# Performance work log

Measured on AMD Instinct MI355X. Metric: run time of the kernel, lower is better.

The kernel has to match this reference:

```python
import jax, jax.numpy as jnp
import numpy as np

EMBED_DIM = 768
Q_DIM = 64
V_DIM = 64
WINDOW_SIZE = 3


def setup_inputs() -> dict:
    key = jax.random.key(0)
    ks = jax.random.split(key, 7)
    B, N = 4, 4096
    s = 1.0 / np.sqrt(EMBED_DIM)
    x = jax.random.normal(ks[0], (B, N, EMBED_DIM), dtype=jnp.float32)
    Wq = jax.random.normal(ks[1], (EMBED_DIM, Q_DIM), dtype=jnp.float32) * s
    bq = jax.random.normal(ks[2], (Q_DIM,), dtype=jnp.float32) * 0.01
    Wk = jax.random.normal(ks[3], (EMBED_DIM, Q_DIM), dtype=jnp.float32) * s
    bk = jax.random.normal(ks[4], (Q_DIM,), dtype=jnp.float32) * 0.01
    Wv = jax.random.normal(ks[5], (EMBED_DIM, V_DIM), dtype=jnp.float32) * s
    bv = jax.random.normal(ks[6], (V_DIM,), dtype=jnp.float32) * 0.01
    return {"x": x, "Wq": Wq, "bq": bq, "Wk": Wk, "bk": bk, "Wv": Wv, "bv": bv}


def reference(x, Wq, bq, Wk, bk, Wv, bv):
    # Faithful translation of SliddingWindowAttention.forward, including the
    # original's quirk: diagonal scores are written into columns 0..window_size-1
    # of a full (B, N, N) zero matrix, softmax is taken over ALL N columns
    # (zeros included), and the result is matmul'd with V.
    B, N, _ = x.shape
    Q = x @ Wq + bq  # (B, N, Q_DIM)
    K = x @ Wk + bk  # (B, N, Q_DIM)
    V = x @ Wv + bv  # (B, N, V_DIM)

    half = WINDOW_SIZE // 2
    columns = jnp.zeros((B, N, N), dtype=x.dtype)
    for idx, di in enumerate(range(-half, half + 1)):
        # diagonal offset di: pair row i with column j = i + di (valid rows only)
        rows = np.arange(max(0, -di), N - max(0, di))
        cols_j = rows + di
        c = jnp.einsum('bid,bid->bi', Q[:, rows, :], K[:, cols_j, :])
        columns = columns.at[:, rows, idx].set(c)

    attn = jax.nn.softmax(columns, axis=2)  # (B, N, N)
    return attn @ V  # (B, N, V_DIM)
```

## Files before the change

### kernel.cpp

```cpp
#include <hip/hip_runtime.h>
#include <hip/hip_bf16.h>
#include <math.h>

#define EMBED 768
#define NTOK  4096
#define NB    4
#define ROWS  16384
#define CN    192

typedef __attribute__((ext_vector_type(8))) short bf16x8;
typedef __attribute__((ext_vector_type(8))) unsigned short u16x8;
typedef __attribute__((ext_vector_type(4))) float f32x4;

__device__ inline void split2(float f, short& h, short& l) {
  union { float f; unsigned u; } a; a.f = f;
  unsigned r = (a.u + 0x7FFFu + ((a.u >> 16) & 1u)) & 0xFFFF0000u;
  h = (short)(r >> 16);
  union { unsigned u; float f; } hf; hf.u = r;
  union { float f; unsigned u; } b; b.f = f - hf.f;
  l = (short)((b.u + 0x7FFFu + ((b.u >> 16) & 1u)) >> 16);
}

__global__ __launch_bounds__(256) void wprep(const float* __restrict__ Wq,
                                             const float* __restrict__ Wk,
                                             const float* __restrict__ Wv,
                                             unsigned short* __restrict__ Wt,
                                             float* __restrict__ Vsum) {
  __shared__ float tile[32 * 64];
  const int b   = blockIdx.x;
  const int mat = b / 24;
  const int ks  = b - mat * 24;
  const float* W = (mat == 0) ? Wq : (mat == 1) ? Wk : Wv;
  const int t = threadIdx.x;

  const float4* src = (const float4*)(W + ks * 2048);
  ((float4*)tile)[t]       = src[t];
  ((float4*)tile)[t + 256] = src[t + 256];
  __syncthreads();

  const int q    = t >> 6;
  const int nloc = t & 63;
  u16x8 hv, lv;
#pragma unroll
  for (int j = 0; j < 8; ++j) {
    short h, l;
    split2(tile[(q * 8 + j) * 64 + nloc], h, l);
    hv[j] = (unsigned short)h;
    lv[j] = (unsigned short)l;
  }
  const size_t base = (size_t)ks * 12288 + (size_t)q * 1536 + (size_t)(mat * 64 + nloc) * 8;
  *(u16x8*)(Wt + base)        = hv;
  *(u16x8*)(Wt + base + 6144) = lv;

  if (b == 0 && t < NB * 64) Vsum[t] = 0.f;
}


__device__ inline void splitHW(float f, short& h, short& l) {
  __hip_bfloat16 hb = __float2bfloat16(f);
  float hf = __bfloat162float(hb);
  __hip_bfloat16 lb = __float2bfloat16(f - hf);
  h = __builtin_bit_cast(short, hb);
  l = __builtin_bit_cast(short, lb);
}

__device__ inline void cvt8hw(const float4 f0, const float4 f1, bf16x8& h, bf16x8& l) {
  short hh, ll;
  splitHW(f0.x, hh, ll); h[0] = hh; l[0] = ll;
  splitHW(f0.y, hh, ll); h[1] = hh; l[1] = ll;
  splitHW(f0.z, hh, ll); h[2] = hh; l[2] = ll;
  splitHW(f0.w, hh, ll); h[3] = hh; l[3] = ll;
  splitHW(f1.x, hh, ll); h[4] = hh; l[4] = ll;
  splitHW(f1.y, hh, ll); h[5] = hh; l[5] = ll;
  splitHW(f1.z, hh, ll); h[6] = hh; l[6] = ll;
  splitHW(f1.w, hh, ll); h[7] = hh; l[7] = ll;
}

__global__ __launch_bounds__(512, 6) void qkv_mfma(const float* __restrict__ x,
                                                   const unsigned short* __restrict__ Wtu,
                                                   const float* __restrict__ bq,
                                                   const float* __restrict__ bk,
                                                   const float* __restrict__ bv,
                                                   float* __restrict__ C,
                                                   float* __restrict__ Vsum) {
  __shared__ float ms[4][16][48];

  const int tid  = threadIdx.x;
  const int lane = tid & 63;
  const int wv   = tid >> 6;
  const int wn   = wv >> 1;
  const int kh   = wv & 1;
  const int ml   = lane & 15;
  const int q    = lane >> 4;
  const int r0   = blockIdx.x * 16;

  f32x4 acc0 = {0.f,0.f,0.f,0.f}, acc1 = {0.f,0.f,0.f,0.f}, acc2 = {0.f,0.f,0.f,0.f};

  const float*          xa = x   + (size_t)(r0 + ml) * EMBED + kh * 384 + q * 8;
  const unsigned short* Bb = Wtu + (size_t)(kh * 12) * 12288 + q * 1536 + (wn * 48 + ml) * 8;

  for (int ks = 0; ks < 12; ++ks) {
    const bf16x8* bp = (const bf16x8*)Bb;
    bf16x8 bh0 = bp[0],  bl0 = bp[768];
    bf16x8 bh1 = bp[16], bl1 = bp[784];
    bf16x8 bh2 = bp[32], bl2 = bp[800];
    float4 a0 = *(const float4*)xa;
    float4 a1 = *(const float4*)(xa + 4);
    bf16x8 ah, al;
    cvt8hw(a0, a1, ah, al);
    acc0 = __builtin_amdgcn_mfma_f32_16x16x32_bf16(ah, bh0, acc0, 0, 0, 0);
    acc1 = __builtin_amdgcn_mfma_f32_16x16x32_bf16(ah, bh1, acc1, 0, 0, 0);
    acc2 = __builtin_amdgcn_mfma_f32_16x16x32_bf16(ah, bh2, acc2, 0, 0, 0);
    acc0 = __builtin_amdgcn_mfma_f32_16x16x32_bf16(ah, bl0, acc0, 0, 0, 0);
    acc1 = __builtin_amdgcn_mfma_f32_16x16x32_bf16(ah, bl1, acc1, 0, 0, 0);
    acc2 = __builtin_amdgcn_mfma_f32_16x16x32_bf16(ah, bl2, acc2, 0, 0, 0);
    acc0 = __builtin_amdgcn_mfma_f32_16x16x32_bf16(al, bh0, acc0, 0, 0, 0);
    acc1 = __builtin_amdgcn_mfma_f32_16x16x32_bf16(al, bh1, acc1, 0, 0, 0);
    acc2 = __builtin_amdgcn_mfma_f32_16x16x32_bf16(al, bh2, acc2, 0, 0, 0);
    xa += 32;
    Bb += 12288;
  }

  if (kh == 1) {
#pragma unroll
    for (int reg = 0; reg < 4; ++reg) {
      ms[wn][q * 4 + reg][0 * 16 + ml] = acc0[reg];
      ms[wn][q * 4 + reg][1 * 16 + ml] = acc1[reg];
      ms[wn][q * 4 + reg][2 * 16 + ml] = acc2[reg];
    }
  }
  __syncthreads();
  if (kh == 1) return;

#pragma unroll
  for (int reg = 0; reg < 4; ++reg) {
    acc0[reg] += ms[wn][q * 4 + reg][0 * 16 + ml];
    acc1[reg] += ms[wn][q * 4 + reg][1 * 16 + ml];
    acc2[reg] += ms[wn][q * 4 + reg][2 * 16 + ml];
  }

#define EPI(NT, ACC) do {                                                   \
    const int n = wn * 48 + (NT) * 16 + ml;                                 \
    const float bias = (n < 64) ? bq[n] : (n < 128) ? bk[n - 64] : bv[n - 128]; \
    const int row = r0 + q * 4;                                             \
    C[(size_t)(row + 0) * CN + n] = ACC[0] + bias;                          \
    C[(size_t)(row + 1) * CN + n] = ACC[1] + bias;                          \
    C[(size_t)(row + 2) * CN + n] = ACC[2] + bias;                          \
    C[(size_t)(row + 3) * CN + n] = ACC[3] + bias;                          \
  } while (0)

  EPI(0, acc0); EPI(1, acc1); EPI(2, acc2);

#define VS(NT, ACC) do {                                                    \
    const int n = wn * 48 + (NT) * 16 + ml;                                 \
    if (n >= 128) {                                                         \
      float s = ACC[0] + ACC[1] + ACC[2] + ACC[3] + 4.f * bv[n - 128];      \
      s += __shfl_xor(s, 16, 64);                                           \
      s += __shfl_xor(s, 32, 64);                                           \
      if (q == 0) atomicAdd(&Vsum[(r0 >> 12) * 64 + (n - 128)], s);         \
    }                                                                       \
  } while (0)

  VS(0, acc0); VS(1, acc1); VS(2, acc2);
}

__global__ __launch_bounds__(256) void attn_kernel(const float* __restrict__ C,
                                                   const float* __restrict__ Vsum,
                                                   float* __restrict__ out) {
  const int t    = threadIdx.x;
  const int lane = t & 63;
  const int wave = t >> 6;
  const int r = blockIdx.x * 4 + wave;
  const int b = r >> 12;
  const int i = r & (NTOK - 1);

  const float q  = C[(size_t)r * CN + lane];
  const float kc = C[(size_t)r * CN + 64 + lane];
  float km = 0.f, kp = 0.f;
  if (i > 0)        km = C[(size_t)(r - 1) * CN + 64 + lane];
  if (i < NTOK - 1) kp = C[(size_t)(r + 1) * CN + 64 + lane];

  float p0 = q * km, p1 = q * kc, p2 = q * kp;
#pragma unroll
  for (int off = 32; off > 0; off >>= 1) {
    p0 += __shfl_xor(p0, off, 64);
    p1 += __shfl_xor(p1, off, 64);
    p2 += __shfl_xor(p2, off, 64);
  }

  const float s0 = (i > 0) ? p0 : 0.f;
  const float s1 = p1;
  const float s2 = (i < NTOK - 1) ? p2 : 0.f;
  const float m  = fmaxf(fmaxf(s0, s1), fmaxf(s2, 0.f));
  const float e0 = expf(s0 - m);
  const float e1 = expf(s1 - m);
  const float e2 = expf(s2 - m);
  const float ez = expf(-m);
  const float Z  = e0 + e1 + e2 + (float)(NTOK - 3) * ez;

  const size_t vb = ((size_t)b * NTOK) * CN + 128;
  const float v0 = C[vb + lane];
  const float v1 = C[vb + CN + lane];
  const float v2 = C[vb + 2 * (size_t)CN + lane];
  const float vs = Vsum[b * 64 + lane];

  out[(size_t)r * 64 + lane] =
      (e0 * v0 + e1 * v1 + e2 * v2 + ez * (vs - v0 - v1 - v2)) / Z;
}

extern "C" void kernel_launch(void* const* d_in, const int* in_sizes, int n_in,
                              void* d_out, int out_size, void* d_ws, size_t ws_size,
                              hipStream_t stream) {
  const float* x  = (const float*)d_in[0];
  const float* Wq = (const float*)d_in[1];
  const float* bq = (const float*)d_in[2];
  const float* Wk = (const float*)d_in[3];
  const float* bk = (const float*)d_in[4];
  const float* Wv = (const float*)d_in[5];
  const float* bv = (const float*)d_in[6];
  float* out = (float*)d_out;

  float* C    = (float*)d_ws;
  float* Vsum = C + (size_t)ROWS * CN;
  unsigned short* Wt = (unsigned short*)(Vsum + NB * 64);

  wprep<<<72, 256, 0, stream>>>(Wq, Wk, Wv, Wt, Vsum);
  qkv_mfma<<<ROWS / 16, 512, 0, stream>>>(x, Wt, bq, bk, bv, C, Vsum);
  attn_kernel<<<ROWS / 4, 256, 0, stream>>>(C, Vsum, out);
}
```

Before: 141.3 us.

## Restructure QKV GEMM as split-K with LDS-staged weights and 32x32 MFMA

The QKV projection is rebuilt as a split-K GEMM. 256 blocks of 1024 threads each handle 256 rows and one quarter of K, and each block stages its weight slice into 144KB of LDS with global_load_lds. The 16x16x32 MFMAs become 32x32x16 MFMAs, and the next x values are prefetched in registers. Partial results are merged with float atomicAdd into a C buffer that wprep now zero-fills, and the Vsum reduction is adapted to the new layout. This aims to cut repeated global weight loads and raise MFMA efficiency, at the cost of many global atomics, an extra zeroing pass, and low occupancy from the large LDS footprint.

```diff
diff --git a/kernel.cpp b/kernel.cpp
--- a/kernel.cpp
+++ b/kernel.cpp
@@ -8,9 +8,9 @@
 #define ROWS  16384
 #define CN    192
 
-typedef __attribute__((ext_vector_type(8))) short bf16x8;
-typedef __attribute__((ext_vector_type(8))) unsigned short u16x8;
-typedef __attribute__((ext_vector_type(4))) float f32x4;
+typedef __attribute__((ext_vector_type(8)))  short bf16x8;
+typedef __attribute__((ext_vector_type(8)))  unsigned short u16x8;
+typedef __attribute__((ext_vector_type(16))) float f32x16;
 
 __device__ inline void split2(float f, short& h, short& l) {
   union { float f; unsigned u; } a; a.f = f;
@@ -25,36 +25,50 @@
                                              const float* __restrict__ Wk,
                                              const float* __restrict__ Wv,
                                              unsigned short* __restrict__ Wt,
-                                             float* __restrict__ Vsum) {
-  __shared__ float tile[32 * 64];
-  const int b   = blockIdx.x;
-  const int mat = b / 24;
-  const int ks  = b - mat * 24;
-  const float* W = (mat == 0) ? Wq : (mat == 1) ? Wk : Wv;
+                                             float* __restrict__ Vsum,
+                                             float* __restrict__ C) {
+  const int b = blockIdx.x;
   const int t = threadIdx.x;
 
-  const float4* src = (const float4*)(W + ks * 2048);
-  ((float4*)tile)[t]       = src[t];
-  ((float4*)tile)[t + 256] = src[t + 256];
-  __syncthreads();
-
-  const int q    = t >> 6;
-  const int nloc = t & 63;
-  u16x8 hv, lv;
+  if (b < 72) {
+    __shared__ float tile[32 * 64];
+    const int mat = b / 24;
+    const int ks  = b - mat * 24;
+    const float* W = (mat == 0) ? Wq : (mat == 1) ? Wk : Wv;
+
+    const float4* src = (const float4*)(W + ks * 2048);
+    ((float4*)tile)[t]       = src[t];
+    ((float4*)tile)[t + 256] = src[t + 256];
+    __syncthreads();
+
+    const int q    = t >> 6;
+    const int nloc = t & 63;
+    u16x8 hv, lv;
 #pragma unroll
-  for (int j = 0; j < 8; ++j) {
-    short h, l;
-    split2(tile[(q * 8 + j) * 64 + nloc], h, l);
-    hv[j] = (unsigned short)h;
-    lv[j] = (unsigned short)l;
-  }
-  const size_t base = (size_t)ks * 12288 + (size_t)q * 1536 + (size_t)(mat * 64 + nloc) * 8;
-  *(u16x8*)(Wt + base)        = hv;
-  *(u16x8*)(Wt + base + 6144) = lv;
-
-  if (b == 0 && t < NB * 64) Vsum[t] = 0.f;
-}
-
+    for (int j = 0; j < 8; ++j) {
+      short h, l;
+      split2(tile[(q * 8 + j) * 64 + nloc], h, l);
+      hv[j] = (unsigned short)h;
+      lv[j] = (unsigned short)l;
+    }
+    const size_t base = (size_t)ks * 12288 + (size_t)q * 1536 + (size_t)(mat * 64 + nloc) * 8;
+    *(u16x8*)(Wt + base)        = hv;
+    *(u16x8*)(Wt + base + 6144) = lv;
+  }
+
+  float4 z; z.x = 0.f; z.y = 0.f; z.z = 0.f; z.w = 0.f;
+  float4* C4 = (float4*)C;
+  for (int i = b * 256 + t; i < 786432; i += 65536) C4[i] = z;
+
+  if (b == 0) Vsum[t] = 0.f;
+}
+
+__device__ inline void gload_lds16(const unsigned short* g, unsigned short* l) {
+  __builtin_amdgcn_global_load_lds(
+      (const __attribute__((address_space(1))) unsigned int*)(g),
+      (__attribute__((address_space(3))) unsigned int*)(l),
+      16, 0, 0);
+}
 
 __device__ inline void splitHW(float f, short& h, short& l) {
   __hip_bfloat16 hb = __float2bfloat16(f);
@@ -76,92 +90,97 @@
   splitHW(f1.w, hh, ll); h[7] = hh; l[7] = ll;
 }
 
-__global__ __launch_bounds__(512, 6) void qkv_mfma(const float* __restrict__ x,
-                                                   const unsigned short* __restrict__ Wtu,
-                                                   const float* __restrict__ bq,
-                                                   const float* __restrict__ bk,
-                                                   const float* __restrict__ bv,
-                                                   float* __restrict__ C,
-                                                   float* __restrict__ Vsum) {
-  __shared__ float ms[4][16][48];
+#define MFMA32(A, B, ACC) \
+  ACC = __builtin_amdgcn_mfma_f32_32x32x16_bf16(A, B, ACC, 0, 0, 0)
+
+__global__ __launch_bounds__(1024, 2) void qkv_mfma(const float* __restrict__ x,
+                                                    const unsigned short* __restrict__ Wtu,
+                                                    const float* __restrict__ bq,
+                                                    const float* __restrict__ bk,
+                                                    const float* __restrict__ bv,
+                                                    float* __restrict__ C,
+                                                    float* __restrict__ Vsum) {
+  extern __shared__ unsigned short lds[];
 
   const int tid  = threadIdx.x;
   const int lane = tid & 63;
-  const int wv   = tid >> 6;
-  const int wn   = wv >> 1;
-  const int kh   = wv & 1;
-  const int ml   = lane & 15;
-  const int q    = lane >> 4;
-  const int r0   = blockIdx.x * 16;
-
-  f32x4 acc0 = {0.f,0.f,0.f,0.f}, acc1 = {0.f,0.f,0.f,0.f}, acc2 = {0.f,0.f,0.f,0.f};
-
-  const float*          xa = x   + (size_t)(r0 + ml) * EMBED + kh * 384 + q * 8;
-  const unsigned short* Bb = Wtu + (size_t)(kh * 12) * 12288 + q * 1536 + (wn * 48 + ml) * 8;
-
-  for (int ks = 0; ks < 12; ++ks) {
-    const bf16x8* bp = (const bf16x8*)Bb;
-    bf16x8 bh0 = bp[0],  bl0 = bp[768];
-    bf16x8 bh1 = bp[16], bl1 = bp[784];
-    bf16x8 bh2 = bp[32], bl2 = bp[800];
-    float4 a0 = *(const float4*)xa;
-    float4 a1 = *(const float4*)(xa + 4);
+  const int wid  = tid >> 6;
+  const int wm   = wid >> 1;
+  const int nb   = (wid & 1) * 96;
+  const int l31  = lane & 31;
+  const int l5   = lane >> 5;
+  const int bid  = blockIdx.x;
+  const int kq   = bid >> 6;
+  const int mc   = bid & 63;
+  const int r0w  = mc * 256 + wm * 32;
+
+  {
+    const unsigned short* g = Wtu + (size_t)kq * 73728 + tid * 8;
+    unsigned short* l = lds + tid * 8;
+#pragma unroll
+    for (int i = 0; i < 9; ++i)
+      gload_lds16(g + i * 8192, l + i * 8192);
+  }
+
+  f32x16 acc0 = {}, acc1 = {}, acc2 = {};
+
+  const float* xa = x + (size_t)(r0w + l31) * EMBED + kq * 192 + l5 * 8;
+  float4 a0 = *(const float4*)xa;
+  float4 a1 = *(const float4*)(xa + 4);
+
+  __syncthreads();
+
+  const unsigned short* lb = lds + nb * 8 + l5 * 1536 + l31 * 8;
+
+  for (int t = 0; t < 12; ++t) {
+    float4 n0, n1;
+    if (t < 11) {
+      n0 = *(const float4*)(xa + 16);
+      n1 = *(const float4*)(xa + 20);
+    }
     bf16x8 ah, al;
     cvt8hw(a0, a1, ah, al);
-    acc0 = __builtin_amdgcn_mfma_f32_16x16x32_bf16(ah, bh0, acc0, 0, 0, 0);
-    acc1 = __builtin_amdgcn_mfma_f32_16x16x32_bf16(ah, bh1, acc1, 0, 0, 0);
-    acc2 = __builtin_amdgcn_mfma_f32_16x16x32_bf16(ah, bh2, acc2, 0, 0, 0);
-    acc0 = __builtin_amdgcn_mfma_f32_16x16x32_bf16(ah, bl0, acc0, 0, 0, 0);
-    acc1 = __builtin_amdgcn_mfma_f32_16x16x32_bf16(ah, bl1, acc1, 0, 0, 0);
-    acc2 = __builtin_amdgcn_mfma_f32_16x16x32_bf16(ah, bl2, acc2, 0, 0, 0);
-    acc0 = __builtin_amdgcn_mfma_f32_16x16x32_bf16(al, bh0, acc0, 0, 0, 0);
-    acc1 = __builtin_amdgcn_mfma_f32_16x16x32_bf16(al, bh1, acc1, 0, 0, 0);
-    acc2 = __builtin_amdgcn_mfma_f32_16x16x32_bf16(al, bh2, acc2, 0, 0, 0);
-    xa += 32;
-    Bb += 12288;
-  }
-
-  if (kh == 1) {
-#pragma unroll
-    for (int reg = 0; reg < 4; ++reg) {
-      ms[wn][q * 4 + reg][0 * 16 + ml] = acc0[reg];
-      ms[wn][q * 4 + reg][1 * 16 + ml] = acc1[reg];
-      ms[wn][q * 4 + reg][2 * 16 + ml] = acc2[reg];
-    }
-  }
-  __syncthreads();
-  if (kh == 1) return;
-
-#pragma unroll
-  for (int reg = 0; reg < 4; ++reg) {
-    acc0[reg] += ms[wn][q * 4 + reg][0 * 16 + ml];
-    acc1[reg] += ms[wn][q * 4 + reg][1 * 16 + ml];
-    acc2[reg] += ms[wn][q * 4 + reg][2 * 16 + ml];
-  }
-
-#define EPI(NT, ACC) do {                                                   \
-    const int n = wn * 48 + (NT) * 16 + ml;                                 \
-    const float bias = (n < 64) ? bq[n] : (n < 128) ? bk[n - 64] : bv[n - 128]; \
-    const int row = r0 + q * 4;                                             \
-    C[(size_t)(row + 0) * CN + n] = ACC[0] + bias;                          \
-    C[(size_t)(row + 1) * CN + n] = ACC[1] + bias;                          \
-    C[(size_t)(row + 2) * CN + n] = ACC[2] + bias;                          \
-    C[(size_t)(row + 3) * CN + n] = ACC[3] + bias;                          \
+    bf16x8 b0h = *(const bf16x8*)(lb);
+    bf16x8 b0l = *(const bf16x8*)(lb + 6144);
+    bf16x8 b1h = *(const bf16x8*)(lb + 256);
+    bf16x8 b1l = *(const bf16x8*)(lb + 6400);
+    bf16x8 b2h = *(const bf16x8*)(lb + 512);
+    bf16x8 b2l = *(const bf16x8*)(lb + 6656);
+    MFMA32(ah, b0h, acc0); MFMA32(ah, b1h, acc1); MFMA32(ah, b2h, acc2);
+    MFMA32(ah, b0l, acc0); MFMA32(ah, b1l, acc1); MFMA32(ah, b2l, acc2);
+    MFMA32(al, b0h, acc0); MFMA32(al, b1h, acc1); MFMA32(al, b2h, acc2);
+    xa += 16;
+    lb += (t & 1) ? 9216 : 3072;
+    a0 = n0; a1 = n1;
+  }
+
+#define EPI32(CT, ACC) do {                                                  \
+    const int col = nb + (CT) * 32 + l31;                                    \
+    float bias = 0.f;                                                        \
+    if (kq == 0)                                                             \
+      bias = (col < 64) ? bq[col] : (col < 128) ? bk[col - 64] : bv[col - 128]; \
+    _Pragma("unroll")                                                        \
+    for (int reg = 0; reg < 16; ++reg) {                                     \
+      const int row = r0w + (reg & 3) + 8 * (reg >> 2) + 4 * l5;             \
+      atomicAdd(&C[(size_t)row * CN + col], ACC[reg] + bias);                \
+    }                                                                        \
   } while (0)
 
-  EPI(0, acc0); EPI(1, acc1); EPI(2, acc2);
-
-#define VS(NT, ACC) do {                                                    \
-    const int n = wn * 48 + (NT) * 16 + ml;                                 \
-    if (n >= 128) {                                                         \
-      float s = ACC[0] + ACC[1] + ACC[2] + ACC[3] + 4.f * bv[n - 128];      \
-      s += __shfl_xor(s, 16, 64);                                           \
-      s += __shfl_xor(s, 32, 64);                                           \
-      if (q == 0) atomicAdd(&Vsum[(r0 >> 12) * 64 + (n - 128)], s);         \
-    }                                                                       \
+  EPI32(0, acc0); EPI32(1, acc1); EPI32(2, acc2);
+
+#define VSUM32(CT, ACC) do {                                                 \
+    const int col = nb + (CT) * 32 + l31;                                    \
+    if (col >= 128) {                                                        \
+      float s = 0.f;                                                         \
+      _Pragma("unroll")                                                      \
+      for (int reg = 0; reg < 16; ++reg) s += ACC[reg];                      \
+      s += __shfl_xor(s, 32, 64);                                            \
+      if (kq == 0) s += 32.f * bv[col - 128];                                \
+      if (lane < 32) atomicAdd(&Vsum[(r0w >> 12) * 64 + (col - 128)], s);    \
+    }                                                                        \
   } while (0)
 
-  VS(0, acc0); VS(1, acc1); VS(2, acc2);
+  VSUM32(1, acc1); VSUM32(2, acc2);
 }
 
 __global__ __launch_bounds__(256) void attn_kernel(const float* __restrict__ C,
@@ -224,7 +243,7 @@
   float* Vsum = C + (size_t)ROWS * CN;
   unsigned short* Wt = (unsigned short*)(Vsum + NB * 64);
 
-  wprep<<<72, 256, 0, stream>>>(Wq, Wk, Wv, Wt, Vsum);
-  qkv_mfma<<<ROWS / 16, 512, 0, stream>>>(x, Wt, bq, bk, bv, C, Vsum);
+  wprep<<<256, 256, 0, stream>>>(Wq, Wk, Wv, Wt, Vsum, C);
+  qkv_mfma<<<256, 1024, 147456, stream>>>(x, Wt, bq, bk, bv, C, Vsum);
   attn_kernel<<<ROWS / 4, 256, 0, stream>>>(C, Vsum, out);
 }
```

New measurement: 158.8 us. 1.12x slower.

## Pre-split x to bf16 hi/lo tiles and stage weights in LDS for GEMM

Applied to the files above, without the earlier changes.

The x-to-bf16 hi/lo split moves into a separate prep kernel that writes MFMA-ready tiles to workspace. The GEMM is retiled so each 512-thread block owns 256 rows by 48 columns, loads its full weight slice (144 KB) into LDS with global_load_lds, and each wave handles two 16-row M tiles with register prefetch of the next K step. This drops the split-K LDS reduction and the per-block conversion of x, and reuses weights across more rows. The cost is an extra full write and read of x in bf16 hi/lo form (about the same bytes as fp32 x), plus lower occupancy and only 256 blocks.

```diff
diff --git a/kernel.cpp b/kernel.cpp
--- a/kernel.cpp
+++ b/kernel.cpp
@@ -12,26 +12,70 @@
 typedef __attribute__((ext_vector_type(8))) unsigned short u16x8;
 typedef __attribute__((ext_vector_type(4))) float f32x4;
 
-__device__ inline void split2(float f, short& h, short& l) {
+struct hl16 { unsigned short h, l; };
+
+__device__ inline hl16 split2(float f) {
+  hl16 r;
   union { float f; unsigned u; } a; a.f = f;
-  unsigned r = (a.u + 0x7FFFu + ((a.u >> 16) & 1u)) & 0xFFFF0000u;
-  h = (short)(r >> 16);
-  union { unsigned u; float f; } hf; hf.u = r;
+  unsigned rr = (a.u + 0x7FFFu + ((a.u >> 16) & 1u)) & 0xFFFF0000u;
+  r.h = (unsigned short)(rr >> 16);
+  union { unsigned u; float f; } hf; hf.u = rr;
   union { float f; unsigned u; } b; b.f = f - hf.f;
-  l = (short)((b.u + 0x7FFFu + ((b.u >> 16) & 1u)) >> 16);
-}
-
-__global__ __launch_bounds__(256) void wprep(const float* __restrict__ Wq,
-                                             const float* __restrict__ Wk,
-                                             const float* __restrict__ Wv,
-                                             unsigned short* __restrict__ Wt,
-                                             float* __restrict__ Vsum) {
+  r.l = (unsigned short)((b.u + 0x7FFFu + ((b.u >> 16) & 1u)) >> 16);
+  return r;
+}
+
+__device__ inline hl16 splitHW(float f) {
+  hl16 r;
+  __hip_bfloat16 hb = __float2bfloat16(f);
+  float hf = __bfloat162float(hb);
+  __hip_bfloat16 lb = __float2bfloat16(f - hf);
+  r.h = __builtin_bit_cast(unsigned short, hb);
+  r.l = __builtin_bit_cast(unsigned short, lb);
+  return r;
+}
+
+__global__ __launch_bounds__(256) void prep(const float* __restrict__ x,
+                                            const float* __restrict__ Wq,
+                                            const float* __restrict__ Wk,
+                                            const float* __restrict__ Wv,
+                                            unsigned short* __restrict__ Wt,
+                                            unsigned short* __restrict__ Xt,
+                                            float* __restrict__ Vsum) {
   __shared__ float tile[32 * 64];
-  const int b   = blockIdx.x;
+  const int bid = blockIdx.x;
+  const int t   = threadIdx.x;
+
+  if (bid < 6144) {
+    const int u   = bid * 4 + (t >> 6);
+    const int mt  = u / 24;
+    const int ks  = u - mt * 24;
+    const int lam = t & 63;
+    const int ml  = lam & 15;
+    const int q   = lam >> 4;
+    const float* src = x + (size_t)(mt * 16 + ml) * EMBED + ks * 32 + q * 8;
+    const float4 a0 = *(const float4*)src;
+    const float4 a1 = *(const float4*)(src + 4);
+    u16x8 hv, lv;
+    hl16 s;
+    s = splitHW(a0.x); hv[0] = s.h; lv[0] = s.l;
+    s = splitHW(a0.y); hv[1] = s.h; lv[1] = s.l;
+    s = splitHW(a0.z); hv[2] = s.h; lv[2] = s.l;
+    s = splitHW(a0.w); hv[3] = s.h; lv[3] = s.l;
+    s = splitHW(a1.x); hv[4] = s.h; lv[4] = s.l;
+    s = splitHW(a1.y); hv[5] = s.h; lv[5] = s.l;
+    s = splitHW(a1.z); hv[6] = s.h; lv[6] = s.l;
+    s = splitHW(a1.w); hv[7] = s.h; lv[7] = s.l;
+    unsigned short* dst = Xt + (size_t)(mt * 24 + ks) * 1024 + lam * 8;
+    *(u16x8*)dst         = hv;
+    *(u16x8*)(dst + 512) = lv;
+    return;
+  }
+
+  const int b   = bid - 6144;
   const int mat = b / 24;
   const int ks  = b - mat * 24;
   const float* W = (mat == 0) ? Wq : (mat == 1) ? Wk : Wv;
-  const int t = threadIdx.x;
 
   const float4* src = (const float4*)(W + ks * 2048);
   ((float4*)tile)[t]       = src[t];
@@ -43,125 +87,118 @@
   u16x8 hv, lv;
 #pragma unroll
   for (int j = 0; j < 8; ++j) {
-    short h, l;
-    split2(tile[(q * 8 + j) * 64 + nloc], h, l);
-    hv[j] = (unsigned short)h;
-    lv[j] = (unsigned short)l;
-  }
-  const size_t base = (size_t)ks * 12288 + (size_t)q * 1536 + (size_t)(mat * 64 + nloc) * 8;
-  *(u16x8*)(Wt + base)        = hv;
-  *(u16x8*)(Wt + base + 6144) = lv;
-
-  if (b == 0 && t < NB * 64) Vsum[t] = 0.f;
-}
-
-
-__device__ inline void splitHW(float f, short& h, short& l) {
-  __hip_bfloat16 hb = __float2bfloat16(f);
-  float hf = __bfloat162float(hb);
-  __hip_bfloat16 lb = __float2bfloat16(f - hf);
-  h = __builtin_bit_cast(short, hb);
-  l = __builtin_bit_cast(short, lb);
-}
-
-__device__ inline void cvt8hw(const float4 f0, const float4 f1, bf16x8& h, bf16x8& l) {
-  short hh, ll;
-  splitHW(f0.x, hh, ll); h[0] = hh; l[0] = ll;
-  splitHW(f0.y, hh, ll); h[1] = hh; l[1] = ll;
-  splitHW(f0.z, hh, ll); h[2] = hh; l[2] = ll;
-  splitHW(f0.w, hh, ll); h[3] = hh; l[3] = ll;
-  splitHW(f1.x, hh, ll); h[4] = hh; l[4] = ll;
-  splitHW(f1.y, hh, ll); h[5] = hh; l[5] = ll;
-  splitHW(f1.z, hh, ll); h[6] = hh; l[6] = ll;
-  splitHW(f1.w, hh, ll); h[7] = hh; l[7] = ll;
-}
-
-__global__ __launch_bounds__(512, 6) void qkv_mfma(const float* __restrict__ x,
+    hl16 s = split2(tile[(q * 8 + j) * 64 + nloc]);
+    hv[j] = s.h; lv[j] = s.l;
+  }
+
+  const int n   = mat * 64 + nloc;
+  const int nqb = n / 48;
+  const int col = n - nqb * 48;
+  unsigned short* dst = Wt + (size_t)nqb * 73728 + (size_t)ks * 3072 + q * 384 + col * 8;
+  *(u16x8*)dst          = hv;
+  *(u16x8*)(dst + 1536) = lv;
+
+  if (b == 0) Vsum[t] = 0.f;
+}
+
+__device__ inline void gload_lds16(const unsigned short* g, unsigned short* l) {
+  __builtin_amdgcn_global_load_lds(
+      (const __attribute__((address_space(1))) unsigned int*)(g),
+      (__attribute__((address_space(3))) unsigned int*)(l),
+      16, 0, 0);
+}
+
+#define MF(A, B, ACC) ACC = __builtin_amdgcn_mfma_f32_16x16x32_bf16(A, B, ACC, 0, 0, 0)
+
+__global__ __launch_bounds__(512, 2) void qkv_mfma(const unsigned short* __restrict__ Xt,
                                                    const unsigned short* __restrict__ Wtu,
                                                    const float* __restrict__ bq,
                                                    const float* __restrict__ bk,
                                                    const float* __restrict__ bv,
                                                    float* __restrict__ C,
                                                    float* __restrict__ Vsum) {
-  __shared__ float ms[4][16][48];
+  extern __shared__ unsigned short lds[];
 
   const int tid  = threadIdx.x;
   const int lane = tid & 63;
-  const int wv   = tid >> 6;
-  const int wn   = wv >> 1;
-  const int kh   = wv & 1;
-  const int ml   = lane & 15;
+  const int wm   = tid >> 6;
+  const int nl   = lane & 15;
   const int q    = lane >> 4;
-  const int r0   = blockIdx.x * 16;
-
-  f32x4 acc0 = {0.f,0.f,0.f,0.f}, acc1 = {0.f,0.f,0.f,0.f}, acc2 = {0.f,0.f,0.f,0.f};
-
-  const float*          xa = x   + (size_t)(r0 + ml) * EMBED + kh * 384 + q * 8;
-  const unsigned short* Bb = Wtu + (size_t)(kh * 12) * 12288 + q * 1536 + (wn * 48 + ml) * 8;
-
-  for (int ks = 0; ks < 12; ++ks) {
-    const bf16x8* bp = (const bf16x8*)Bb;
-    bf16x8 bh0 = bp[0],  bl0 = bp[768];
-    bf16x8 bh1 = bp[16], bl1 = bp[784];
-    bf16x8 bh2 = bp[32], bl2 = bp[800];
-    float4 a0 = *(const float4*)xa;
-    float4 a1 = *(const float4*)(xa + 4);
-    bf16x8 ah, al;
-    cvt8hw(a0, a1, ah, al);
-    acc0 = __builtin_amdgcn_mfma_f32_16x16x32_bf16(ah, bh0, acc0, 0, 0, 0);
-    acc1 = __builtin_amdgcn_mfma_f32_16x16x32_bf16(ah, bh1, acc1, 0, 0, 0);
-    acc2 = __builtin_amdgcn_mfma_f32_16x16x32_bf16(ah, bh2, acc2, 0, 0, 0);
-    acc0 = __builtin_amdgcn_mfma_f32_16x16x32_bf16(ah, bl0, acc0, 0, 0, 0);
-    acc1 = __builtin_amdgcn_mfma_f32_16x16x32_bf16(ah, bl1, acc1, 0, 0, 0);
-    acc2 = __builtin_amdgcn_mfma_f32_16x16x32_bf16(ah, bl2, acc2, 0, 0, 0);
-    acc0 = __builtin_amdgcn_mfma_f32_16x16x32_bf16(al, bh0, acc0, 0, 0, 0);
-    acc1 = __builtin_amdgcn_mfma_f32_16x16x32_bf16(al, bh1, acc1, 0, 0, 0);
-    acc2 = __builtin_amdgcn_mfma_f32_16x16x32_bf16(al, bh2, acc2, 0, 0, 0);
-    xa += 32;
-    Bb += 12288;
-  }
-
-  if (kh == 1) {
+  const int bid  = blockIdx.x;
+  const int mc   = (bid & 7) * 8 + (bid >> 5);
+  const int nqb  = (bid >> 3) & 3;
+  const int nbase = nqb * 48;
+  const int r0w  = mc * 256 + wm * 32;
+  const int mt0  = mc * 16 + wm * 2;
+
+  {
+    const unsigned short* g = Wtu + (size_t)nqb * 73728 + tid * 8;
+    unsigned short* l = lds + tid * 8;
 #pragma unroll
-    for (int reg = 0; reg < 4; ++reg) {
-      ms[wn][q * 4 + reg][0 * 16 + ml] = acc0[reg];
-      ms[wn][q * 4 + reg][1 * 16 + ml] = acc1[reg];
-      ms[wn][q * 4 + reg][2 * 16 + ml] = acc2[reg];
+    for (int i = 0; i < 18; ++i)
+      gload_lds16(g + i * 4096, l + i * 4096);
+  }
+
+  f32x4 acc00 = {0.f,0.f,0.f,0.f}, acc01 = {0.f,0.f,0.f,0.f}, acc02 = {0.f,0.f,0.f,0.f};
+  f32x4 acc10 = {0.f,0.f,0.f,0.f}, acc11 = {0.f,0.f,0.f,0.f}, acc12 = {0.f,0.f,0.f,0.f};
+
+  const bf16x8* XA0 = (const bf16x8*)Xt + (size_t)mt0 * 3072 + lane;
+  const bf16x8* XA1 = XA0 + 3072;
+
+  bf16x8 ah0 = XA0[0], al0 = XA0[64];
+  bf16x8 ah1 = XA1[0], al1 = XA1[64];
+
+  __syncthreads();
+
+  const bf16x8* LB = (const bf16x8*)lds + q * 48 + nl;
+
+  for (int ks = 0; ks < 24; ++ks) {
+    const int o = ks * 384;
+    bf16x8 bh0 = LB[o],       bh1 = LB[o + 16],  bh2 = LB[o + 32];
+    bf16x8 bl0 = LB[o + 192], bl1 = LB[o + 208], bl2 = LB[o + 224];
+    bf16x8 nh0, nl0, nh1, nl1;
+    if (ks < 23) {
+      nh0 = XA0[(ks + 1) * 128]; nl0 = XA0[(ks + 1) * 128 + 64];
+      nh1 = XA1[(ks + 1) * 128]; nl1 = XA1[(ks + 1) * 128 + 64];
     }
-  }
-  __syncthreads();
-  if (kh == 1) return;
-
-#pragma unroll
-  for (int reg = 0; reg < 4; ++reg) {
-    acc0[reg] += ms[wn][q * 4 + reg][0 * 16 + ml];
-    acc1[reg] += ms[wn][q * 4 + reg][1 * 16 + ml];
-    acc2[reg] += ms[wn][q * 4 + reg][2 * 16 + ml];
-  }
-
-#define EPI(NT, ACC) do {                                                   \
-    const int n = wn * 48 + (NT) * 16 + ml;                                 \
-    const float bias = (n < 64) ? bq[n] : (n < 128) ? bk[n - 64] : bv[n - 128]; \
-    const int row = r0 + q * 4;                                             \
-    C[(size_t)(row + 0) * CN + n] = ACC[0] + bias;                          \
-    C[(size_t)(row + 1) * CN + n] = ACC[1] + bias;                          \
-    C[(size_t)(row + 2) * CN + n] = ACC[2] + bias;                          \
-    C[(size_t)(row + 3) * CN + n] = ACC[3] + bias;                          \
+    MF(ah0, bh0, acc00); MF(ah1, bh0, acc10);
+    MF(ah0, bh1, acc01); MF(ah1, bh1, acc11);
+    MF(ah0, bh2, acc02); MF(ah1, bh2, acc12);
+    MF(ah0, bl0, acc00); MF(ah1, bl0, acc10);
+    MF(ah0, bl1, acc01); MF(ah1, bl1, acc11);
+    MF(ah0, bl2, acc02); MF(ah1, bl2, acc12);
+    MF(al0, bh0, acc00); MF(al1, bh0, acc10);
+    MF(al0, bh1, acc01); MF(al1, bh1, acc11);
+    MF(al0, bh2, acc02); MF(al1, bh2, acc12);
+    ah0 = nh0; al0 = nl0; ah1 = nh1; al1 = nl1;
+  }
+
+#define EPI(MI, NT, ACC) do {                                               \
+    const int col = nbase + (NT) * 16 + nl;                                 \
+    const float bias = (col < 64) ? bq[col]                                 \
+                     : (col < 128) ? bk[col - 64] : bv[col - 128];          \
+    const int row = r0w + (MI) * 16 + q * 4;                                \
+    C[(size_t)(row + 0) * CN + col] = ACC[0] + bias;                        \
+    C[(size_t)(row + 1) * CN + col] = ACC[1] + bias;                        \
+    C[(size_t)(row + 2) * CN + col] = ACC[2] + bias;                        \
+    C[(size_t)(row + 3) * CN + col] = ACC[3] + bias;                        \
   } while (0)
 
-  EPI(0, acc0); EPI(1, acc1); EPI(2, acc2);
-
-#define VS(NT, ACC) do {                                                    \
-    const int n = wn * 48 + (NT) * 16 + ml;                                 \
-    if (n >= 128) {                                                         \
-      float s = ACC[0] + ACC[1] + ACC[2] + ACC[3] + 4.f * bv[n - 128];      \
+  EPI(0, 0, acc00); EPI(0, 1, acc01); EPI(0, 2, acc02);
+  EPI(1, 0, acc10); EPI(1, 1, acc11); EPI(1, 2, acc12);
+
+#define VS(NT, A0, A1) do {                                                 \
+    const int col = nbase + (NT) * 16 + nl;                                 \
+    if (col >= 128) {                                                       \
+      float s = A0[0] + A0[1] + A0[2] + A0[3]                               \
+              + A1[0] + A1[1] + A1[2] + A1[3] + 8.f * bv[col - 128];        \
       s += __shfl_xor(s, 16, 64);                                           \
       s += __shfl_xor(s, 32, 64);                                           \
-      if (q == 0) atomicAdd(&Vsum[(r0 >> 12) * 64 + (n - 128)], s);         \
+      if (q == 0) atomicAdd(&Vsum[(r0w >> 12) * 64 + (col - 128)], s);      \
     }                                                                       \
   } while (0)
 
-  VS(0, acc0); VS(1, acc1); VS(2, acc2);
+  VS(0, acc00, acc10); VS(1, acc01, acc11); VS(2, acc02, acc12);
 }
 
 __global__ __launch_bounds__(256) void attn_kernel(const float* __restrict__ C,
@@ -223,8 +260,9 @@
   float* C    = (float*)d_ws;
   float* Vsum = C + (size_t)ROWS * CN;
   unsigned short* Wt = (unsigned short*)(Vsum + NB * 64);
-
-  wprep<<<72, 256, 0, stream>>>(Wq, Wk, Wv, Wt, Vsum);
-  qkv_mfma<<<ROWS / 16, 512, 0, stream>>>(x, Wt, bq, bk, bv, C, Vsum);
+  unsigned short* Xt = Wt + 4 * 73728;
+
+  prep<<<6216, 256, 0, stream>>>(x, Wq, Wk, Wv, Wt, Xt, Vsum);
+  qkv_mfma<<<256, 512, 147456, stream>>>(Xt, Wt, bq, bk, bv, C, Vsum);
   attn_kernel<<<ROWS / 4, 256, 0, stream>>>(C, Vsum, out);
 }
```

Result: faster. 127.5 us (-9.8%).
